# Optimization experiments

Measured on AMD Instinct MI355X. Metric: run time of the kernel, lower is better.

The kernel has to match this reference:

```python
import jax, jax.numpy as jnp
import numpy as np

DIM = 512
NUM_HEADS = 8
HEAD_DIM = DIM // NUM_HEADS
EPS = 1e-12  # F.normalize default eps


def _l2norm(x):
    # F.normalize: x / max(||x||_2, eps) along last dim
    n = jnp.sqrt(jnp.sum(x * x, axis=-1, keepdims=True))
    return x / jnp.maximum(n, EPS)


def setup_inputs() -> dict:
    key = jax.random.key(0)
    ks = jax.random.split(key, 7)
    B, N, K = 8, 4096, 256
    scale = 1.0 / np.sqrt(DIM)
    return {
        "X_flat": jax.random.normal(ks[0], (B, N, DIM), jnp.float32),
        "S_tokens": jax.random.normal(ks[1], (B, K, DIM), jnp.float32),
        "Wq": jax.random.normal(ks[2], (DIM, DIM), jnp.float32) * scale,
        "Wk": jax.random.normal(ks[3], (DIM, DIM), jnp.float32) * scale,
        "Wv": jax.random.normal(ks[4], (DIM, DIM), jnp.float32) * scale,
        "Wo": jax.random.normal(ks[5], (DIM, DIM), jnp.float32) * scale,
        "temperature": jnp.ones((NUM_HEADS, 1, 1), jnp.float32),
    }


def reference(X_flat, S_tokens, Wq, Wk, Wv, Wo, temperature):
    B, N, C = X_flat.shape
    K = S_tokens.shape[1]
    H, D = NUM_HEADS, HEAD_DIM
    # torch Linear: y = x @ W.T
    q = (X_flat @ Wq.T).reshape(B, N, H, D).transpose(0, 2, 1, 3)   # (B,H,N,D)
    k = (S_tokens @ Wk.T).reshape(B, K, H, D).transpose(0, 2, 1, 3)  # (B,H,K,D)
    v = (S_tokens @ Wv.T).reshape(B, K, H, D).transpose(0, 2, 1, 3)  # (B,H,K,D)
    q = _l2norm(q)
    k = _l2norm(k)
    attn = jnp.einsum('bhnd,bhkd->bhnk', q, k) * temperature  # temperature (H,1,1) broadcasts
    attn = jax.nn.softmax(attn, axis=-1)
    out = jnp.einsum('bhnk,bhkd->bhnd', attn, v)
    out = out.transpose(0, 2, 1, 3).reshape(B, N, C)
    out = out @ Wo.T
    return X_flat + out
```

## Files before the change

kernel.cpp:

```cpp
#include <hip/hip_runtime.h>
#include <hip/hip_bf16.h>


typedef __bf16 bf16;
typedef __attribute__((ext_vector_type(8))) __bf16 bf16x8;
typedef __attribute__((ext_vector_type(4))) float f32x4;

#if __has_builtin(__builtin_amdgcn_exp2f)
#define EXP2(x) __builtin_amdgcn_exp2f(x)
#else
#define EXP2(x) exp2f(x)
#endif

__device__ __forceinline__ void gload_lds16(const void* g, void* l) {
  __builtin_amdgcn_global_load_lds(
      (__attribute__((address_space(1))) void*)g,
      (__attribute__((address_space(3))) void*)l, 16, 0, 0);
}

__device__ __forceinline__ unsigned pack2(float a, float b) {
  unsigned short x = __builtin_bit_cast(unsigned short, (bf16)a);
  unsigned short y = __builtin_bit_cast(unsigned short, (bf16)b);
  return (unsigned)x | ((unsigned)y << 16);
}

__global__ __launch_bounds__(256) void cvt_all(
    const float* __restrict__ X, const float* __restrict__ S,
    const float* __restrict__ Wq, const float* __restrict__ Wk,
    const float* __restrict__ Wv, const float* __restrict__ Wo,
    bf16* __restrict__ Xb, bf16* __restrict__ Sb, bf16* __restrict__ Wqb,
    bf16* __restrict__ Wkb, bf16* __restrict__ Wvb, bf16* __restrict__ Wob) {
  int i = blockIdx.x * 256 + threadIdx.x;
  const float* src;
  bf16* dst;
  int r;
  if (i < 2097152) {
    src = X; dst = Xb; r = i;
  } else if (i < 2228224) {
    src = S; dst = Sb; r = i - 2097152;
  } else {
    int j = i - 2228224;
    int w = j >> 15;
    r = j & 32767;
    src = (w == 0) ? Wq : (w == 1) ? Wk : (w == 2) ? Wv : Wo;
    dst = (w == 0) ? Wqb : (w == 1) ? Wkb : (w == 2) ? Wvb : Wob;
  }
  float4 a = *(const float4*)(src + (size_t)r * 8);
  float4 b = *(const float4*)(src + (size_t)r * 8 + 4);
  uint4 v;
  v.x = pack2(a.x, a.y);
  v.y = pack2(a.z, a.w);
  v.z = pack2(b.x, b.y);
  v.w = pack2(b.z, b.w);
  *(uint4*)(dst + (size_t)r * 8) = v;
}

__global__ __launch_bounds__(256) void proj_all(
    const bf16* __restrict__ Xb, const bf16* __restrict__ Sb,
    const bf16* __restrict__ Wqb, const bf16* __restrict__ Wkb,
    const bf16* __restrict__ Wvb, const float* __restrict__ temp,
    bf16* __restrict__ Q, bf16* __restrict__ Kn, bf16* __restrict__ Vt) {
  __shared__ __align__(16) char smem[49152];

  const int lg = (blockIdx.x & 7) * 144 + (blockIdx.x >> 3);

  const bf16* A;
  const bf16* W;
  int m0, kind;
  if (lg < 1024) {
    kind = 0; A = Xb; W = Wqb; m0 = (lg >> 2) * 128;
  } else if (lg < 1088) {
    kind = 1; A = Sb; W = Wkb; m0 = ((lg - 1024) >> 2) * 128;
  } else {
    kind = 2; A = Sb; W = Wvb; m0 = ((lg - 1088) >> 2) * 128;
  }
  const int n0 = (lg & 3) * 128;

  const int tid = threadIdx.x;
  const int wid = tid >> 6, lane = tid & 63;
  const int wr = wid >> 1, wc = wid & 1;
  const int g = lane >> 4, c16 = lane & 15;
  const int r0 = tid >> 2, cc0 = tid & 3;
  const int r1 = (256 + tid) >> 2, cc1 = tid & 3;
  const int dst0 = (tid & ~63) * 16, dst1 = (256 + (tid & ~63)) * 16;

  f32x4 acc[4][4] = {};

#define PSTAGE(kb, buf)                                                     \
  {                                                                         \
    char* as = smem + (buf) * 8192;                                         \
    char* bs = smem + 24576 + (buf) * 8192;                                 \
    gload_lds16(A + (size_t)(m0 + r0) * 512 + (kb) + cc0 * 8, as + dst0);   \
    gload_lds16(A + (size_t)(m0 + r1) * 512 + (kb) + cc1 * 8, as + dst1);   \
    gload_lds16(W + (size_t)(n0 + r0) * 512 + (kb) + cc0 * 8, bs + dst0);   \
    gload_lds16(W + (size_t)(n0 + r1) * 512 + (kb) + cc1 * 8, bs + dst1);   \
  }

#define PCOMPUTE(buf)                                                       \
  {                                                                         \
    const bf16* as = (const bf16*)(smem + (buf) * 8192);                    \
    const bf16* bs = (const bf16*)(smem + 24576 + (buf) * 8192);            \
    bf16x8 af[4], bfr[4];                                                   \
    _Pragma("unroll") for (int mi = 0; mi < 4; ++mi) af[mi] =               \
        *(const bf16x8*)(as + (wr * 64 + mi * 16 + c16) * 32 + g * 8);      \
    _Pragma("unroll") for (int ni = 0; ni < 4; ++ni) bfr[ni] =              \
        *(const bf16x8*)(bs + (wc * 64 + ni * 16 + c16) * 32 + g * 8);      \
    _Pragma("unroll") for (int mi = 0; mi < 4; ++mi)                        \
        _Pragma("unroll") for (int ni = 0; ni < 4; ++ni) acc[mi][ni] =      \
            __builtin_amdgcn_mfma_f32_16x16x32_bf16(af[mi], bfr[ni],        \
                                                    acc[mi][ni], 0, 0, 0);  \
  }

  PSTAGE(0, 0);
  PSTAGE(32, 1);
  int bufc = 0;
  for (int t = 0; t < 14; ++t) {
    int bufn = bufc + 2;
    if (bufn >= 3) bufn -= 3;
    PSTAGE((t + 2) * 32, bufn);
    asm volatile("s_waitcnt vmcnt(8)" ::: "memory");
    __builtin_amdgcn_s_barrier();
    PCOMPUTE(bufc);
    __builtin_amdgcn_s_barrier();
    if (++bufc == 3) bufc = 0;
  }
  asm volatile("s_waitcnt vmcnt(4)" ::: "memory");
  __builtin_amdgcn_s_barrier();
  PCOMPUTE(bufc);
  __builtin_amdgcn_s_barrier();
  if (++bufc == 3) bufc = 0;
  asm volatile("s_waitcnt vmcnt(0)" ::: "memory");
  __builtin_amdgcn_s_barrier();
  PCOMPUTE(bufc);

  __syncthreads();

  if (kind != 2) {
    bf16* C = (kind == 0) ? Q : Kn;
    const float sc =
        (kind == 0) ? temp[(n0 + wc * 64) >> 6] * 1.44269504088896f : 1.0f;
    char* eps = smem + wid * 8192;
#pragma unroll
    for (int mi = 0; mi < 4; ++mi) {
      float ss[4];
#pragma unroll
      for (int j = 0; j < 4; ++j) {
        float s = 0.f;
#pragma unroll
        for (int ni = 0; ni < 4; ++ni) {
          float v = acc[mi][ni][j];
          s += v * v;
        }
        ss[j] = s;
      }
#pragma unroll
      for (int msk = 1; msk < 16; msk <<= 1)
#pragma unroll
        for (int j = 0; j < 4; ++j) ss[j] += __shfl_xor(ss[j], msk, 64);
      float inv[4];
#pragma unroll
      for (int j = 0; j < 4; ++j)
        inv[j] = rsqrtf(fmaxf(ss[j], 1e-24f)) * sc;
#pragma unroll
      for (int ni = 0; ni < 4; ++ni)
#pragma unroll
        for (int j = 0; j < 4; ++j) {
          int row = mi * 16 + g * 4 + j, col = ni * 16 + c16;
          int off = (row * 128 + col * 2) ^ ((row & 7) << 4);
          *(bf16*)(eps + off) = (bf16)(acc[mi][ni][j] * inv[j]);
        }
    }
    asm volatile("s_waitcnt lgkmcnt(0)" ::: "memory");
#pragma unroll
    for (int it = 0; it < 8; ++it) {
      int c = it * 64 + lane;
      int row = c >> 3, ch = c & 7;
      int off = (row * 128 + ch * 16) ^ ((row & 7) << 4);
      bf16x8 v = *(const bf16x8*)(eps + off);
      *(bf16x8*)(C + (size_t)(m0 + wr * 64 + row) * 512 + n0 + wc * 64 +
                 ch * 8) = v;
    }
  } else {
#pragma unroll
    for (int mi = 0; mi < 4; ++mi) {
      int m = m0 + wr * 64 + mi * 16 + g * 4;
      int b = m >> 8, tt = m & 255;
#pragma unroll
      for (int ni = 0; ni < 4; ++ni) {
        int col = n0 + wc * 64 + ni * 16 + c16;
        int h = col >> 6, d = col & 63;
        uint2 v;
        v.x = pack2(acc[mi][ni][0], acc[mi][ni][1]);
        v.y = pack2(acc[mi][ni][2], acc[mi][ni][3]);
        *(uint2*)(Vt + ((size_t)((b * 8 + h) * 64 + d) * 256 + tt)) = v;
      }
    }
  }
#undef PSTAGE
#undef PCOMPUTE
}

__global__ __launch_bounds__(256) void out_gemm(
    const bf16* __restrict__ O, const bf16* __restrict__ Wob,
    const float* __restrict__ Xres, float* __restrict__ out) {
  __shared__ __align__(16) char smem[49152];

  const int lg = (blockIdx.x & 7) * 128 + (blockIdx.x >> 3);
  const int m0 = (lg >> 2) * 128, n0 = (lg & 3) * 128;

  const int tid = threadIdx.x;
  const int wid = tid >> 6, lane = tid & 63;
  const int wr = wid >> 1, wc = wid & 1;
  const int g = lane >> 4, c16 = lane & 15;
  const int r0 = tid >> 2, cc0 = tid & 3;
  const int r1 = (256 + tid) >> 2, cc1 = tid & 3;
  const int dst0 = (tid & ~63) * 16, dst1 = (256 + (tid & ~63)) * 16;

  f32x4 acc[4][4] = {};

#define OSTAGE(kb, buf)                                                      \
  {                                                                          \
    char* as = smem + (buf) * 8192;                                          \
    char* bs = smem + 24576 + (buf) * 8192;                                  \
    gload_lds16(O + (size_t)(m0 + r0) * 512 + (kb) + cc0 * 8, as + dst0);    \
    gload_lds16(O + (size_t)(m0 + r1) * 512 + (kb) + cc1 * 8, as + dst1);    \
    gload_lds16(Wob + (size_t)(n0 + r0) * 512 + (kb) + cc0 * 8, bs + dst0);  \
    gload_lds16(Wob + (size_t)(n0 + r1) * 512 + (kb) + cc1 * 8, bs + dst1);  \
  }

#define OCOMPUTE(buf)                                                       \
  {                                                                         \
    const bf16* as = (const bf16*)(smem + (buf) * 8192);                    \
    const bf16* bs = (const bf16*)(smem + 24576 + (buf) * 8192);            \
    bf16x8 af[4], bfr[4];                                                   \
    _Pragma("unroll") for (int mi = 0; mi < 4; ++mi) af[mi] =               \
        *(const bf16x8*)(as + (wr * 64 + mi * 16 + c16) * 32 + g * 8);      \
    _Pragma("unroll") for (int ni = 0; ni < 4; ++ni) bfr[ni] =              \
        *(const bf16x8*)(bs + (wc * 64 + ni * 16 + c16) * 32 + g * 8);      \
    _Pragma("unroll") for (int mi = 0; mi < 4; ++mi)                        \
        _Pragma("unroll") for (int ni = 0; ni < 4; ++ni) acc[mi][ni] =      \
            __builtin_amdgcn_mfma_f32_16x16x32_bf16(af[mi], bfr[ni],        \
                                                    acc[mi][ni], 0, 0, 0);  \
  }

  OSTAGE(0, 0);
  OSTAGE(32, 1);
  int bufc = 0;
  for (int t = 0; t < 14; ++t) {
    int bufn = bufc + 2;
    if (bufn >= 3) bufn -= 3;
    OSTAGE((t + 2) * 32, bufn);
    asm volatile("s_waitcnt vmcnt(8)" ::: "memory");
    __builtin_amdgcn_s_barrier();
    OCOMPUTE(bufc);
    __builtin_amdgcn_s_barrier();
    if (++bufc == 3) bufc = 0;
  }
  asm volatile("s_waitcnt vmcnt(4)" ::: "memory");
  __builtin_amdgcn_s_barrier();
  OCOMPUTE(bufc);
  __builtin_amdgcn_s_barrier();
  if (++bufc == 3) bufc = 0;
  asm volatile("s_waitcnt vmcnt(0)" ::: "memory");
  __builtin_amdgcn_s_barrier();
  OCOMPUTE(bufc);

  __syncthreads();

  char* eps = smem + wid * 8192;
#pragma unroll
  for (int p = 0; p < 2; ++p) {
#pragma unroll
    for (int mm = 0; mm < 2; ++mm)
#pragma unroll
      for (int ni = 0; ni < 4; ++ni)
#pragma unroll
        for (int j = 0; j < 4; ++j) {
          int row = mm * 16 + g * 4 + j, col = ni * 16 + c16;
          int off = (row * 256 + col * 4) ^ ((row & 7) << 4);
          *(float*)(eps + off) = acc[p * 2 + mm][ni][j];
        }
    asm volatile("s_waitcnt lgkmcnt(0)" ::: "memory");
#pragma unroll
    for (int it = 0; it < 8; ++it) {
      int c = it * 64 + lane;
      int row = c >> 4, ch = c & 15;
      int off = (row * 256 + ch * 16) ^ ((row & 7) << 4);
      float4 v = *(const float4*)(eps + off);
      size_t gr = (size_t)(m0 + wr * 64 + p * 32 + row) * 512 + n0 +
                  wc * 64 + ch * 4;
      float4 x = *(const float4*)(Xres + gr);
      v.x += x.x;
      v.y += x.y;
      v.z += x.z;
      v.w += x.w;
      *(float4*)(out + gr) = v;
    }
    asm volatile("s_waitcnt lgkmcnt(0)" ::: "memory");
  }
#undef OSTAGE
#undef OCOMPUTE
}

__global__ __launch_bounds__(256) void attn_fused(
    const bf16* __restrict__ Qn, const bf16* __restrict__ Kn,
    const bf16* __restrict__ Vt, bf16* __restrict__ O) {
  __shared__ __align__(16) char smem[65536];

  const int tid = threadIdx.x;
  const int w = tid >> 6, lane = tid & 63;
  const int g = lane >> 4, c16 = lane & 15;
  const int lg = (blockIdx.x & 7) * 512 + (blockIdx.x >> 3);
  const int nt = lg & 63, h = (lg >> 6) & 7, b = lg >> 9;
  const int n0 = nt * 64;

  {
    const bf16* Ksrc = Kn + ((size_t)b * 256) * 512 + h * 64;
    const bf16* Vsrc = Vt + (size_t)((b * 8 + h) * 64) * 256;
#pragma unroll
    for (int it = 0; it < 8; ++it) {
      int base = it * 256 + w * 64;
      int c = base + lane;
      int t = c >> 3, dk = (c & 7) ^ (t & 7);
      gload_lds16(Ksrc + (size_t)t * 512 + dk * 8, smem + base * 16);
      int d = c >> 5, tc = (c & 31) ^ (d & 7);
      gload_lds16(Vsrc + (size_t)d * 256 + tc * 8, smem + 32768 + base * 16);
    }
  }
  const int q = w * 16 + c16;
  const bf16* Qsrc = Qn + ((size_t)b * 4096 + n0) * 512 + h * 64;
  bf16x8 qf[2];
  qf[0] = *(const bf16x8*)(Qsrc + (size_t)q * 512 + g * 8);
  qf[1] = *(const bf16x8*)(Qsrc + (size_t)q * 512 + 32 + g * 8);
  __syncthreads();

  f32x4 sacc[16] = {};
#pragma unroll
  for (int mi = 0; mi < 16; ++mi) {
#pragma unroll
    for (int s = 0; s < 2; ++s) {
      int t = mi * 16 + c16;
      int off = (t * 128 + s * 64 + g * 16) ^ ((t & 7) << 4);
      bf16x8 kf = *(const bf16x8*)(smem + off);
      sacc[mi] = __builtin_amdgcn_mfma_f32_16x16x32_bf16(kf, qf[s], sacc[mi],
                                                         0, 0, 0);
    }
  }

  float mx4[4] = {-1e30f, -1e30f, -1e30f, -1e30f};
#pragma unroll
  for (int mi = 0; mi < 16; ++mi)
#pragma unroll
    for (int j = 0; j < 4; ++j) mx4[j] = fmaxf(mx4[j], sacc[mi][j]);
  float mx = fmaxf(fmaxf(mx4[0], mx4[1]), fmaxf(mx4[2], mx4[3]));
  mx = fmaxf(mx, __shfl_xor(mx, 16, 64));
  mx = fmaxf(mx, __shfl_xor(mx, 32, 64));
  float sm4[4] = {0.f, 0.f, 0.f, 0.f};
#pragma unroll
  for (int mi = 0; mi < 16; ++mi)
#pragma unroll
    for (int j = 0; j < 4; ++j) {
      float p = EXP2(sacc[mi][j] - mx);
      sacc[mi][j] = p;
      sm4[j] += p;
    }
  float sum = (sm4[0] + sm4[1]) + (sm4[2] + sm4[3]);
  sum += __shfl_xor(sum, 16, 64);
  sum += __shfl_xor(sum, 32, 64);
  float inv = 1.0f / sum;

  __syncthreads();

#pragma unroll
  for (int mi = 0; mi < 16; ++mi) {
    uint2 v;
    v.x = pack2(sacc[mi][0], sacc[mi][1]);
    v.y = pack2(sacc[mi][2], sacc[mi][3]);
    int off = (q * 512 + mi * 32 + g * 8) ^ ((q & 7) << 4);
    *(uint2*)(smem + off) = v;
  }

  f32x4 oacc[4] = {};
#pragma unroll
  for (int ks = 0; ks < 8; ++ks) {
    int offa = (q * 512 + ks * 64 + g * 16) ^ ((q & 7) << 4);
    bf16x8 pa = *(const bf16x8*)(smem + offa);
#pragma unroll
    for (int ni = 0; ni < 4; ++ni) {
      int d = ni * 16 + c16;
      int offb = 32768 + ((d * 512 + ks * 64 + g * 16) ^ ((d & 7) << 4));
      bf16x8 vb = *(const bf16x8*)(smem + offb);
      oacc[ni] = __builtin_amdgcn_mfma_f32_16x16x32_bf16(pa, vb, oacc[ni],
                                                         0, 0, 0);
    }
  }

  {
    char* ox = smem + w * 8192;
#pragma unroll
    for (int ni = 0; ni < 4; ++ni)
#pragma unroll
      for (int j = 0; j < 4; ++j) {
        int row = g * 4 + j, col = ni * 16 + c16;
        int off = (row * 128 + col * 2) ^ ((row & 7) << 4);
        *(bf16*)(ox + off) = (bf16)(oacc[ni][j] * inv);
      }
    asm volatile("s_waitcnt lgkmcnt(0)" ::: "memory");
#pragma unroll
    for (int it = 0; it < 2; ++it) {
      int c = it * 64 + lane;
      int row = c >> 3, ch = c & 7;
      int off = (row * 128 + ch * 16) ^ ((row & 7) << 4);
      bf16x8 v = *(const bf16x8*)(ox + off);
      *(bf16x8*)(O + ((size_t)b * 4096 + n0 + w * 16 + row) * 512 + h * 64 +
                 ch * 8) = v;
    }
  }
}

extern "C" void kernel_launch(void* const* d_in, const int* in_sizes, int n_in,
                              void* d_out, int out_size, void* d_ws,
                              size_t ws_size, hipStream_t stream) {
  const float* X = (const float*)d_in[0];
  const float* S = (const float*)d_in[1];
  const float* Wq = (const float*)d_in[2];
  const float* Wk = (const float*)d_in[3];
  const float* Wv = (const float*)d_in[4];
  const float* Wo = (const float*)d_in[5];
  const float* temp = (const float*)d_in[6];
  float* out = (float*)d_out;

  char* ws = (char*)d_ws;
  bf16* Qws = (bf16*)ws;
  bf16* Kws = (bf16*)(ws + 33554432);
  bf16* Vtws = (bf16*)(ws + 35651584);
  bf16* Wqb = (bf16*)(ws + 37748736);
  bf16* Wkb = (bf16*)(ws + 38273024);
  bf16* Wvb = (bf16*)(ws + 38797312);
  bf16* Wob = (bf16*)(ws + 39321600);

  bf16* Xb = (bf16*)d_out;
  bf16* Sb = (bf16*)((char*)d_out + 33554432);

  cvt_all<<<dim3(9216), dim3(256), 0, stream>>>(X, S, Wq, Wk, Wv, Wo, Xb, Sb,
                                                Wqb, Wkb, Wvb, Wob);
  proj_all<<<dim3(1152), dim3(256), 0, stream>>>(Xb, Sb, Wqb, Wkb, Wvb, temp,
                                                 Qws, Kws, Vtws);
  attn_fused<<<dim3(4096), dim3(256), 0, stream>>>(Qws, Kws, Vtws, Qws);
  out_gemm<<<dim3(1024), dim3(256), 0, stream>>>(Qws, Wob, X, out);
}
```

Before: 127.6 us.

## Process 128 query rows per attention block and pre-layout K/V in MFMA fragment order

Each attention block now handles two 64-row query tiles against the same K/V loaded into LDS, halving the grid and the redundant K/V global loads per block. K and V are staged into LDS already arranged in MFMA fragment order, so the fragment reads become linear without XOR swizzles. P is written to a per-wave LDS slice instead of a block-wide buffer, and each tile's PV product is done sequentially with explicit waits. The cost is doubled score accumulator registers (two sets of 16 f32x4), which may lower occupancy, and fewer blocks in flight.

Result: slower. 148.3 us (+16.2%).

```diff
diff --git a/kernel.cpp b/kernel.cpp
--- a/kernel.cpp
+++ b/kernel.cpp
@@ -310,9 +310,9 @@
   const int tid = threadIdx.x;
   const int w = tid >> 6, lane = tid & 63;
   const int g = lane >> 4, c16 = lane & 15;
-  const int lg = (blockIdx.x & 7) * 512 + (blockIdx.x >> 3);
-  const int nt = lg & 63, h = (lg >> 6) & 7, b = lg >> 9;
-  const int n0 = nt * 64;
+  const int lg = (blockIdx.x & 7) * 256 + (blockIdx.x >> 3);
+  const int nt = lg & 31, h = (lg >> 5) & 7, b = lg >> 8;
+  const int n0 = nt * 128;
 
   {
     const bf16* Ksrc = Kn + ((size_t)b * 256) * 512 + h * 64;
@@ -321,101 +321,128 @@
     for (int it = 0; it < 8; ++it) {
       int base = it * 256 + w * 64;
       int c = base + lane;
-      int t = c >> 3, dk = (c & 7) ^ (t & 7);
-      gload_lds16(Ksrc + (size_t)t * 512 + dk * 8, smem + base * 16);
-      int d = c >> 5, tc = (c & 31) ^ (d & 7);
-      gload_lds16(Vsrc + (size_t)d * 256 + tc * 8, smem + 32768 + base * 16);
-    }
-  }
-  const int q = w * 16 + c16;
+      int ii = c >> 6, rr = c & 63;
+      int fc16 = rr >> 2, fg = rr & 3;
+      int kmi = ii >> 1, ks_ = ii & 1;
+      gload_lds16(Ksrc + (size_t)(kmi * 16 + fc16) * 512 + ks_ * 32 + fg * 8,
+                  smem + base * 16);
+      int vks = ii >> 2, vni = ii & 3;
+      gload_lds16(Vsrc + (size_t)(vni * 16 + fc16) * 256 + vks * 32 + fg * 8,
+                  smem + 32768 + base * 16);
+    }
+  }
   const bf16* Qsrc = Qn + ((size_t)b * 4096 + n0) * 512 + h * 64;
-  bf16x8 qf[2];
-  qf[0] = *(const bf16x8*)(Qsrc + (size_t)q * 512 + g * 8);
-  qf[1] = *(const bf16x8*)(Qsrc + (size_t)q * 512 + 32 + g * 8);
+  bf16x8 qf0[2], qf1[2];
+  {
+    const bf16* q0 = Qsrc + (size_t)(w * 16 + c16) * 512;
+    const bf16* q1 = Qsrc + (size_t)(64 + w * 16 + c16) * 512;
+    qf0[0] = *(const bf16x8*)(q0 + g * 8);
+    qf0[1] = *(const bf16x8*)(q0 + 32 + g * 8);
+    qf1[0] = *(const bf16x8*)(q1 + g * 8);
+    qf1[1] = *(const bf16x8*)(q1 + 32 + g * 8);
+  }
   __syncthreads();
 
-  f32x4 sacc[16] = {};
+  f32x4 sacc0[16] = {}, sacc1[16] = {};
 #pragma unroll
   for (int mi = 0; mi < 16; ++mi) {
 #pragma unroll
     for (int s = 0; s < 2; ++s) {
-      int t = mi * 16 + c16;
-      int off = (t * 128 + s * 64 + g * 16) ^ ((t & 7) << 4);
-      bf16x8 kf = *(const bf16x8*)(smem + off);
-      sacc[mi] = __builtin_amdgcn_mfma_f32_16x16x32_bf16(kf, qf[s], sacc[mi],
-                                                         0, 0, 0);
-    }
-  }
-
-  float mx4[4] = {-1e30f, -1e30f, -1e30f, -1e30f};
+      bf16x8 kf =
+          *(const bf16x8*)(smem + ((mi * 2 + s) * 64 + c16 * 4 + g) * 16);
+      sacc0[mi] = __builtin_amdgcn_mfma_f32_16x16x32_bf16(kf, qf0[s],
+                                                          sacc0[mi], 0, 0, 0);
+      sacc1[mi] = __builtin_amdgcn_mfma_f32_16x16x32_bf16(kf, qf1[s],
+                                                          sacc1[mi], 0, 0, 0);
+    }
+  }
+
+  float mxa[4] = {-1e30f, -1e30f, -1e30f, -1e30f};
+  float mxb[4] = {-1e30f, -1e30f, -1e30f, -1e30f};
 #pragma unroll
   for (int mi = 0; mi < 16; ++mi)
 #pragma unroll
-    for (int j = 0; j < 4; ++j) mx4[j] = fmaxf(mx4[j], sacc[mi][j]);
-  float mx = fmaxf(fmaxf(mx4[0], mx4[1]), fmaxf(mx4[2], mx4[3]));
-  mx = fmaxf(mx, __shfl_xor(mx, 16, 64));
-  mx = fmaxf(mx, __shfl_xor(mx, 32, 64));
-  float sm4[4] = {0.f, 0.f, 0.f, 0.f};
+    for (int j = 0; j < 4; ++j) {
+      mxa[j] = fmaxf(mxa[j], sacc0[mi][j]);
+      mxb[j] = fmaxf(mxb[j], sacc1[mi][j]);
+    }
+  float mx0 = fmaxf(fmaxf(mxa[0], mxa[1]), fmaxf(mxa[2], mxa[3]));
+  float mx1 = fmaxf(fmaxf(mxb[0], mxb[1]), fmaxf(mxb[2], mxb[3]));
+  mx0 = fmaxf(mx0, __shfl_xor(mx0, 16, 64));
+  mx0 = fmaxf(mx0, __shfl_xor(mx0, 32, 64));
+  mx1 = fmaxf(mx1, __shfl_xor(mx1, 16, 64));
+  mx1 = fmaxf(mx1, __shfl_xor(mx1, 32, 64));
+  float sa[4] = {0.f, 0.f, 0.f, 0.f}, sb[4] = {0.f, 0.f, 0.f, 0.f};
 #pragma unroll
   for (int mi = 0; mi < 16; ++mi)
 #pragma unroll
     for (int j = 0; j < 4; ++j) {
-      float p = EXP2(sacc[mi][j] - mx);
-      sacc[mi][j] = p;
-      sm4[j] += p;
-    }
-  float sum = (sm4[0] + sm4[1]) + (sm4[2] + sm4[3]);
-  sum += __shfl_xor(sum, 16, 64);
-  sum += __shfl_xor(sum, 32, 64);
-  float inv = 1.0f / sum;
+      float p0 = EXP2(sacc0[mi][j] - mx0);
+      float p1 = EXP2(sacc1[mi][j] - mx1);
+      sacc0[mi][j] = p0;
+      sacc1[mi][j] = p1;
+      sa[j] += p0;
+      sb[j] += p1;
+    }
+  float sum0 = (sa[0] + sa[1]) + (sa[2] + sa[3]);
+  float sum1 = (sb[0] + sb[1]) + (sb[2] + sb[3]);
+  sum0 += __shfl_xor(sum0, 16, 64);
+  sum0 += __shfl_xor(sum0, 32, 64);
+  sum1 += __shfl_xor(sum1, 16, 64);
+  sum1 += __shfl_xor(sum1, 32, 64);
+  float inv0 = 1.0f / sum0, inv1 = 1.0f / sum1;
 
   __syncthreads();
 
-#pragma unroll
-  for (int mi = 0; mi < 16; ++mi) {
-    uint2 v;
-    v.x = pack2(sacc[mi][0], sacc[mi][1]);
-    v.y = pack2(sacc[mi][2], sacc[mi][3]);
-    int off = (q * 512 + mi * 32 + g * 8) ^ ((q & 7) << 4);
-    *(uint2*)(smem + off) = v;
-  }
-
-  f32x4 oacc[4] = {};
-#pragma unroll
-  for (int ks = 0; ks < 8; ++ks) {
-    int offa = (q * 512 + ks * 64 + g * 16) ^ ((q & 7) << 4);
-    bf16x8 pa = *(const bf16x8*)(smem + offa);
-#pragma unroll
-    for (int ni = 0; ni < 4; ++ni) {
-      int d = ni * 16 + c16;
-      int offb = 32768 + ((d * 512 + ks * 64 + g * 16) ^ ((d & 7) << 4));
-      bf16x8 vb = *(const bf16x8*)(smem + offb);
-      oacc[ni] = __builtin_amdgcn_mfma_f32_16x16x32_bf16(pa, vb, oacc[ni],
-                                                         0, 0, 0);
-    }
-  }
-
-  {
-    char* ox = smem + w * 8192;
-#pragma unroll
-    for (int ni = 0; ni < 4; ++ni)
-#pragma unroll
-      for (int j = 0; j < 4; ++j) {
-        int row = g * 4 + j, col = ni * 16 + c16;
-        int off = (row * 128 + col * 2) ^ ((row & 7) << 4);
-        *(bf16*)(ox + off) = (bf16)(oacc[ni][j] * inv);
-      }
-    asm volatile("s_waitcnt lgkmcnt(0)" ::: "memory");
-#pragma unroll
-    for (int it = 0; it < 2; ++it) {
-      int c = it * 64 + lane;
-      int row = c >> 3, ch = c & 7;
-      int off = (row * 128 + ch * 16) ^ ((row & 7) << 4);
-      bf16x8 v = *(const bf16x8*)(ox + off);
-      *(bf16x8*)(O + ((size_t)b * 4096 + n0 + w * 16 + row) * 512 + h * 64 +
-                 ch * 8) = v;
-    }
-  }
+  char* pslice = smem + w * 8192;
+
+#define DO_PV(SACC, INV, P)                                                  \
+  {                                                                          \
+    _Pragma("unroll") for (int mi = 0; mi < 16; ++mi) {                      \
+      int cl = (mi >> 1) * 64 + c16 * 4 + ((mi & 1) * 2 + (g >> 1));         \
+      uint2 v;                                                               \
+      v.x = pack2(SACC[mi][0], SACC[mi][1]);                                 \
+      v.y = pack2(SACC[mi][2], SACC[mi][3]);                                 \
+      *(uint2*)(pslice + cl * 16 + (g & 1) * 8) = v;                         \
+    }                                                                        \
+    asm volatile("s_waitcnt lgkmcnt(0)" ::: "memory");                       \
+    __builtin_amdgcn_sched_barrier(0);                                       \
+    f32x4 oacc[4] = {};                                                      \
+    _Pragma("unroll") for (int ks = 0; ks < 8; ++ks) {                       \
+      bf16x8 pa =                                                            \
+          *(const bf16x8*)(pslice + (ks * 64 + c16 * 4 + g) * 16);           \
+      _Pragma("unroll") for (int ni = 0; ni < 4; ++ni) {                     \
+        bf16x8 vb = *(const bf16x8*)(                                        \
+            smem + 32768 + ((ks * 4 + ni) * 64 + c16 * 4 + g) * 16);         \
+        oacc[ni] = __builtin_amdgcn_mfma_f32_16x16x32_bf16(pa, vb,           \
+                                                           oacc[ni], 0,0,0); \
+      }                                                                      \
+    }                                                                        \
+    asm volatile("s_waitcnt lgkmcnt(0)" ::: "memory");                       \
+    __builtin_amdgcn_sched_barrier(0);                                       \
+    _Pragma("unroll") for (int ni = 0; ni < 4; ++ni)                         \
+        _Pragma("unroll") for (int j = 0; j < 4; ++j) {                      \
+      int row = g * 4 + j, col = ni * 16 + c16;                              \
+      int off = (row * 128 + col * 2) ^ ((row & 7) << 4);                    \
+      *(bf16*)(pslice + off) = (bf16)(oacc[ni][j] * (INV));                  \
+    }                                                                        \
+    asm volatile("s_waitcnt lgkmcnt(0)" ::: "memory");                       \
+    __builtin_amdgcn_sched_barrier(0);                                       \
+    _Pragma("unroll") for (int it = 0; it < 2; ++it) {                       \
+      int c = it * 64 + lane;                                                \
+      int row = c >> 3, ch = c & 7;                                          \
+      int off = (row * 128 + ch * 16) ^ ((row & 7) << 4);                    \
+      bf16x8 v = *(const bf16x8*)(pslice + off);                             \
+      *(bf16x8*)(O + ((size_t)b * 4096 + n0 + (P) * 64 + w * 16 + row) *     \
+                         512 + h * 64 + ch * 8) = v;                         \
+    }                                                                        \
+    asm volatile("s_waitcnt lgkmcnt(0)" ::: "memory");                       \
+    __builtin_amdgcn_sched_barrier(0);                                       \
+  }
+
+  DO_PV(sacc0, inv0, 0);
+  DO_PV(sacc1, inv1, 1);
+#undef DO_PV
 }
 
 extern "C" void kernel_launch(void* const* d_in, const int* in_sizes, int n_in,
@@ -446,6 +473,6 @@
                                                 Wqb, Wkb, Wvb, Wob);
   proj_all<<<dim3(1152), dim3(256), 0, stream>>>(Xb, Sb, Wqb, Wkb, Wvb, temp,
                                                  Qws, Kws, Vtws);
-  attn_fused<<<dim3(4096), dim3(256), 0, stream>>>(Qws, Kws, Vtws, Qws);
+  attn_fused<<<dim3(2048), dim3(256), 0, stream>>>(Qws, Kws, Vtws, Qws);
   out_gemm<<<dim3(1024), dim3(256), 0, stream>>>(Qws, Wob, X, out);
 }
```

## Store K, V and P in LDS in MFMA fragment order for linear per-lane reads

Applied to the files above, without the earlier changes.

K and V tiles are now written into LDS already permuted into MFMA operand fragment order, so each lane reads one contiguous 16-byte chunk per fragment with no XOR swizzle address math. The P matrix is moved into a per-wave LDS slice, also in fragment order, and explicit waitcnt and sched barriers are added between the phases. This is meant to cut LDS address arithmetic and bank conflicts in the attention kernel. The global loads for K and V become less contiguous per wave, and the barriers limit how the compiler can overlap the phases.

Measured after the change: 131.8 us. 1.03x slower.

```diff
diff --git a/kernel.cpp b/kernel.cpp
--- a/kernel.cpp
+++ b/kernel.cpp
@@ -321,10 +321,14 @@
     for (int it = 0; it < 8; ++it) {
       int base = it * 256 + w * 64;
       int c = base + lane;
-      int t = c >> 3, dk = (c & 7) ^ (t & 7);
-      gload_lds16(Ksrc + (size_t)t * 512 + dk * 8, smem + base * 16);
-      int d = c >> 5, tc = (c & 31) ^ (d & 7);
-      gload_lds16(Vsrc + (size_t)d * 256 + tc * 8, smem + 32768 + base * 16);
+      int ii = c >> 6, rr = c & 63;
+      int fc16 = rr & 15, fg = rr >> 4;
+      int kmi = ii >> 1, ks_ = ii & 1;
+      gload_lds16(Ksrc + (size_t)(kmi * 16 + fc16) * 512 + ks_ * 32 + fg * 8,
+                  smem + base * 16);
+      int vks = ii >> 2, vni = ii & 3;
+      gload_lds16(Vsrc + (size_t)(vni * 16 + fc16) * 256 + vks * 32 + fg * 8,
+                  smem + 32768 + base * 16);
     }
   }
   const int q = w * 16 + c16;
@@ -339,9 +343,7 @@
   for (int mi = 0; mi < 16; ++mi) {
 #pragma unroll
     for (int s = 0; s < 2; ++s) {
-      int t = mi * 16 + c16;
-      int off = (t * 128 + s * 64 + g * 16) ^ ((t & 7) << 4);
-      bf16x8 kf = *(const bf16x8*)(smem + off);
+      bf16x8 kf = *(const bf16x8*)(smem + ((mi * 2 + s) * 64 + lane) * 16);
       sacc[mi] = __builtin_amdgcn_mfma_f32_16x16x32_bf16(kf, qf[s], sacc[mi],
                                                          0, 0, 0);
     }
@@ -371,47 +373,50 @@
 
   __syncthreads();
 
+  char* pslice = smem + w * 8192;
 #pragma unroll
   for (int mi = 0; mi < 16; ++mi) {
+    int un = (mi >> 1) * 64 + ((mi & 1) * 2 + (g >> 1)) * 16 + c16;
     uint2 v;
     v.x = pack2(sacc[mi][0], sacc[mi][1]);
     v.y = pack2(sacc[mi][2], sacc[mi][3]);
-    int off = (q * 512 + mi * 32 + g * 8) ^ ((q & 7) << 4);
-    *(uint2*)(smem + off) = v;
-  }
+    *(uint2*)(pslice + un * 16 + (g & 1) * 8) = v;
+  }
+  asm volatile("s_waitcnt lgkmcnt(0)" ::: "memory");
+  __builtin_amdgcn_sched_barrier(0);
 
   f32x4 oacc[4] = {};
 #pragma unroll
   for (int ks = 0; ks < 8; ++ks) {
-    int offa = (q * 512 + ks * 64 + g * 16) ^ ((q & 7) << 4);
-    bf16x8 pa = *(const bf16x8*)(smem + offa);
+    bf16x8 pa = *(const bf16x8*)(pslice + (ks * 64 + lane) * 16);
 #pragma unroll
     for (int ni = 0; ni < 4; ++ni) {
-      int d = ni * 16 + c16;
-      int offb = 32768 + ((d * 512 + ks * 64 + g * 16) ^ ((d & 7) << 4));
-      bf16x8 vb = *(const bf16x8*)(smem + offb);
+      bf16x8 vb =
+          *(const bf16x8*)(smem + 32768 + ((ks * 4 + ni) * 64 + lane) * 16);
       oacc[ni] = __builtin_amdgcn_mfma_f32_16x16x32_bf16(pa, vb, oacc[ni],
                                                          0, 0, 0);
     }
   }
+  asm volatile("s_waitcnt lgkmcnt(0)" ::: "memory");
+  __builtin_amdgcn_sched_barrier(0);
 
   {
-    char* ox = smem + w * 8192;
 #pragma unroll
     for (int ni = 0; ni < 4; ++ni)
 #pragma unroll
       for (int j = 0; j < 4; ++j) {
         int row = g * 4 + j, col = ni * 16 + c16;
         int off = (row * 128 + col * 2) ^ ((row & 7) << 4);
-        *(bf16*)(ox + off) = (bf16)(oacc[ni][j] * inv);
+        *(bf16*)(pslice + off) = (bf16)(oacc[ni][j] * inv);
       }
     asm volatile("s_waitcnt lgkmcnt(0)" ::: "memory");
+    __builtin_amdgcn_sched_barrier(0);
 #pragma unroll
     for (int it = 0; it < 2; ++it) {
       int c = it * 64 + lane;
       int row = c >> 3, ch = c & 7;
       int off = (row * 128 + ch * 16) ^ ((row & 7) << 4);
-      bf16x8 v = *(const bf16x8*)(ox + off);
+      bf16x8 v = *(const bf16x8*)(pslice + off);
       *(bf16x8*)(O + ((size_t)b * 4096 + n0 + w * 16 + row) * 512 + h * 64 +
                  ch * 8) = v;
     }
```
